# Kernel optimization log

Hardware: AMD Instinct MI355X
Metric: run time of the kernel (lower is better)

Reference implementation:

```python
import jax, jax.numpy as jnp
import numpy as np

N = 100000   # nodes per type
E = 400000   # edges per relation
D = 128      # in_dim == out_dim
H = 4        # heads
DK = D // H  # 32
EPS = 1e-5


def setup_inputs() -> dict:
    key = jax.random.key(0)
    ks = jax.random.split(key, 16)
    s = 1.0 / np.sqrt(D)  # fan-in scaling for stable activations
    inp = {
        "x_drug": jax.random.normal(ks[0], (N, D), jnp.float32),
        "x_dis": jax.random.normal(ks[1], (N, D), jnp.float32),
        "Wp_drug": jax.random.normal(ks[2], (D, D), jnp.float32) * s,
        "bp_drug": jnp.zeros((D,), jnp.float32),
        "Wp_dis": jax.random.normal(ks[3], (D, D), jnp.float32) * s,
        "bp_dis": jnp.zeros((D,), jnp.float32),
        "Wk_r0": jax.random.normal(ks[4], (D, D), jnp.float32) * s,
        "Wv_r0": jax.random.normal(ks[5], (D, D), jnp.float32) * s,
        "Wk_r1": jax.random.normal(ks[6], (D, D), jnp.float32) * s,
        "Wv_r1": jax.random.normal(ks[7], (D, D), jnp.float32) * s,
        "Wu_drug": jax.random.normal(ks[8], (D, D), jnp.float32) * s,
        "bu_drug": jnp.zeros((D,), jnp.float32),
        "Wu_dis": jax.random.normal(ks[9], (D, D), jnp.float32) * s,
        "bu_dis": jnp.zeros((D,), jnp.float32),
        "g_drug": jnp.ones((D,), jnp.float32),
        "be_drug": jnp.zeros((D,), jnp.float32),
        "g_dis": jnp.ones((D,), jnp.float32),
        "be_dis": jnp.zeros((D,), jnp.float32),
        "ei_r0": jax.random.randint(ks[10], (2, E), 0, N, jnp.int32),  # drug -> dis
        "ei_r1": jax.random.randint(ks[11], (2, E), 0, N, jnp.int32),  # dis  -> drug
    }
    return inp


def _rel_attention(h_src_all, h_dst_all, ei, Wk, Wv, n_dst):
    # gather -> per-relation K/V proj -> edge softmax over dst -> scatter-add
    src, dst = ei[0], ei[1]
    h_src = h_src_all[src]                                  # [E, D]
    Q = h_dst_all[dst].reshape(-1, H, DK)                   # [E, H, DK]
    K = (h_src @ Wk).reshape(-1, H, DK)
    V = (h_src @ Wv).reshape(-1, H, DK)
    scores = jnp.sum(Q * K, axis=-1) / np.sqrt(DK)          # [E, H]
    # scatter_softmax over destination groups (numerically stable)
    m = jax.lax.stop_gradient(
        jax.ops.segment_max(scores, dst, num_segments=n_dst))  # [N, H]
    ex = jnp.exp(scores - m[dst])
    ssum = jax.ops.segment_sum(ex, dst, num_segments=n_dst)    # [N, H]
    attn = ex / ssum[dst]                                      # [E, H]
    wV = (V * attn[..., None]).reshape(-1, D)                  # [E, D]
    return jax.ops.segment_sum(wV, dst, num_segments=n_dst)    # [N, D]


def _update(h, agg, Wu, bu, g, be):
    x = h + (agg @ Wu + bu)  # skip + update (dropout=0)
    mu = jnp.mean(x, axis=-1, keepdims=True)
    var = jnp.var(x, axis=-1, keepdims=True)
    ln = (x - mu) * jax.lax.rsqrt(var + EPS) * g + be
    return jax.nn.relu(ln)


def reference(x_drug, x_dis, Wp_drug, bp_drug, Wp_dis, bp_dis,
              Wk_r0, Wv_r0, Wk_r1, Wv_r1,
              Wu_drug, bu_drug, Wu_dis, bu_dis,
              g_drug, be_drug, g_dis, be_dis, ei_r0, ei_r1):
    # type-specific projection
    h_drug = x_drug @ Wp_drug + bp_drug
    h_dis = x_dis @ Wp_dis + bp_dis
    # per-relation attention + intra/inter-type aggregation
    agg_dis = _rel_attention(h_drug, h_dis, ei_r0, Wk_r0, Wv_r0, N)
    agg_drug = _rel_attention(h_dis, h_drug, ei_r1, Wk_r1, Wv_r1, N)
    out_drug = _update(h_drug, agg_drug, Wu_drug, bu_drug, g_drug, be_drug)
    out_dis = _update(h_dis, agg_dis, Wu_dis, bu_dis, g_dis, be_dis)
    return jnp.stack([out_drug, out_dis])  # [2, N, D]
```

## Files before the change

kernel.cpp:

```cpp
#include <hip/hip_runtime.h>
#include <math.h>

#define NN 100000
#define EE 400000
#define DD 128

typedef __attribute__((ext_vector_type(8))) short bf16x8;
typedef __attribute__((ext_vector_type(4))) float f32x4;

#if defined(__has_builtin)
#if __has_builtin(__builtin_amdgcn_fdot2_f32_bf16)
#define HAVE_FDOT2 1
typedef __attribute__((ext_vector_type(2))) __bf16 bf16x2t;
#endif
#endif

__device__ __forceinline__ unsigned short f2bf(float f) {
  unsigned u = __float_as_uint(f);
  u += 0x7FFF + ((u >> 16) & 1);
  return (unsigned short)(u >> 16);
}
__device__ __forceinline__ float bf2f(unsigned short u) {
  return __uint_as_float(((unsigned)u) << 16);
}

__global__ __launch_bounds__(256) void prep_weights(
    const float* __restrict__ Wp_dr, const float* __restrict__ bp_dr,
    const float* __restrict__ Wp_di, const float* __restrict__ bp_di,
    const float* __restrict__ Wu_dr, const float* __restrict__ Wu_di,
    const float* __restrict__ Bk0, const float* __restrict__ Bv0,
    const float* __restrict__ Bk1, const float* __restrict__ Bv1,
    unsigned short* __restrict__ Wpt_dr, unsigned short* __restrict__ Wpt_di,
    unsigned short* __restrict__ Wut_dr, unsigned short* __restrict__ Wut_di,
    unsigned short* __restrict__ Wkt0, float* __restrict__ bk0,
    unsigned short* __restrict__ Wvt0, float* __restrict__ bv0,
    unsigned short* __restrict__ Wkt1, float* __restrict__ bk1,
    unsigned short* __restrict__ Wvt1, float* __restrict__ bv1) {
  const int b = blockIdx.x, t = threadIdx.x;
  if (b < 256) {
    const int id = b * 256 + t;
    const int m = id >> 14, rem = id & 16383, k = rem & 127, c = rem >> 7;
    const float* W = (m == 0) ? Wp_dr : (m == 1) ? Wp_di : (m == 2) ? Wu_dr : Wu_di;
    unsigned short* O = (m == 0) ? Wpt_dr : (m == 1) ? Wpt_di : (m == 2) ? Wut_dr : Wut_di;
    O[c * DD + k] = f2bf(W[(size_t)k * DD + c]);
  } else if (b < 512) {
    const int id = (b - 256) * 256 + t;
    const int m = id >> 14, rem = id & 16383, k = rem & 127, c = rem >> 7;
    const float* A = (m < 2) ? Wp_dr : Wp_di;
    const float* B = (m == 0) ? Bk0 : (m == 1) ? Bv0 : (m == 2) ? Bk1 : Bv1;
    unsigned short* O = (m == 0) ? Wkt0 : (m == 1) ? Wvt0 : (m == 2) ? Wkt1 : Wvt1;
    const float4* a4 = (const float4*)(A + (size_t)k * DD);
    float s = 0.0f;
#pragma unroll 8
    for (int j4 = 0; j4 < 32; ++j4) {
      const float4 av = a4[j4];
      s += av.x * B[(4 * j4 + 0) * DD + c] + av.y * B[(4 * j4 + 1) * DD + c]
         + av.z * B[(4 * j4 + 2) * DD + c] + av.w * B[(4 * j4 + 3) * DD + c];
    }
    O[c * DD + k] = f2bf(s);
  } else {
    const int id = (b - 512) * 256 + t;
    if (id < 512) {
      const int m = id >> 7, c = id & 127;
      const float* bp = (m < 2) ? bp_dr : bp_di;
      const float* B = (m == 0) ? Bk0 : (m == 1) ? Bv0 : (m == 2) ? Bk1 : Bv1;
      float* bo = (m == 0) ? bk0 : (m == 1) ? bv0 : (m == 2) ? bk1 : bv1;
      float s = 0.0f;
#pragma unroll 8
      for (int j = 0; j < DD; ++j) s += bp[j] * B[j * DD + c];
      bo[c] = s;
    }
  }
}

__device__ __forceinline__ void proj_phase(
    const unsigned short* __restrict__ Wt, const float* __restrict__ bias,
    unsigned short* __restrict__ outg, unsigned short* WL, unsigned short* OT,
    const bf16x8* a, int tid, int lane, int wid, int rb) {
  __syncthreads();
#pragma unroll
  for (int i = tid; i < 2048; i += 256) {
    const int L = i * 16;
    *(float4*)((char*)WL + (L ^ (((L >> 8) & 7) << 4))) = ((const float4*)Wt)[i];
  }
  __syncthreads();
  const int lr0 = (lane >> 4) * 4;
  const int trow = wid * 16 + lr0;
#pragma unroll
  for (int ni = 0; ni < 8; ++ni) {
    const int cl = ni * 16 + (lane & 15);
    f32x4 acc = {0.f, 0.f, 0.f, 0.f};
#pragma unroll
    for (int kk = 0; kk < 4; ++kk) {
      int boff = cl * 256 + kk * 64 + (lane >> 4) * 16;
      boff ^= (cl & 7) << 4;
      const bf16x8 bb = *(const bf16x8*)((const char*)WL + boff);
      acc = __builtin_amdgcn_mfma_f32_16x16x32_bf16(a[kk], bb, acc, 0, 0, 0);
    }
    const float bv = bias[cl];
#pragma unroll
    for (int r = 0; r < 4; ++r)
      OT[(trow + r) * DD + cl] = f2bf(acc[r] + bv);
  }
  __syncthreads();
#pragma unroll
  for (int it = 0; it < 4; ++it) {
    const int row = it * 16 + (tid >> 4), c = (tid & 15) * 8;
    if (rb + row < NN)
      *(uint4*)(outg + (size_t)(rb + row) * DD + c) = *(const uint4*)(OT + row * DD + c);
  }
}

__global__ __launch_bounds__(256) void fused_proj(
    const float* __restrict__ x0, const unsigned short* __restrict__ Wpt0,
    const float* __restrict__ bp0, const unsigned short* __restrict__ Wkta,
    const float* __restrict__ bka, const unsigned short* __restrict__ Wvta,
    const float* __restrict__ bva, unsigned short* __restrict__ h0,
    unsigned short* __restrict__ K0, unsigned short* __restrict__ V0,
    const float* __restrict__ x1, const unsigned short* __restrict__ Wpt1,
    const float* __restrict__ bp1, const unsigned short* __restrict__ Wktb,
    const float* __restrict__ bkb, const unsigned short* __restrict__ Wvtb,
    const float* __restrict__ bvb, unsigned short* __restrict__ h1,
    unsigned short* __restrict__ K1, unsigned short* __restrict__ V1, int half) {
  __shared__ unsigned short WL[DD * DD];
  __shared__ unsigned short AL[64 * DD];
  __shared__ unsigned short OT[64 * DD];
  int bid = blockIdx.x;
  const bool second = bid >= half;
  if (second) bid -= half;
  const float* x = second ? x1 : x0;
  const unsigned short* Wpt = second ? Wpt1 : Wpt0;
  const float* bpv = second ? bp1 : bp0;
  const unsigned short* Wkt = second ? Wktb : Wkta;
  const float* bkv = second ? bkb : bka;
  const unsigned short* Wvt = second ? Wvtb : Wvta;
  const float* bvv = second ? bvb : bva;
  unsigned short* h = second ? h1 : h0;
  unsigned short* K = second ? K1 : K0;
  unsigned short* V = second ? V1 : V0;

  const int tid = threadIdx.x, lane = tid & 63, wid = tid >> 6;
  const int rb = bid * 64;
#pragma unroll
  for (int it = 0; it < 8; ++it) {
    const int r = it * 8 + (tid >> 5), c = (tid & 31) * 4;
    unsigned long long pk = 0;
    if (rb + r < NN) {
      const float4 f = *(const float4*)(x + (size_t)(rb + r) * DD + c);
      pk = (unsigned long long)f2bf(f.x) | ((unsigned long long)f2bf(f.y) << 16)
         | ((unsigned long long)f2bf(f.z) << 32) | ((unsigned long long)f2bf(f.w) << 48);
    }
    int L = r * 256 + c * 2;
    L ^= (r & 7) << 4;
    *(unsigned long long*)((char*)AL + L) = pk;
  }
  __syncthreads();
  bf16x8 a[4];
  {
    const int ar = wid * 16 + (lane & 15);
#pragma unroll
    for (int kk = 0; kk < 4; ++kk) {
      int L = ar * 256 + kk * 64 + (lane >> 4) * 16;
      L ^= (ar & 7) << 4;
      a[kk] = *(const bf16x8*)((const char*)AL + L);
    }
  }
  proj_phase(Wpt, bpv, h, WL, OT, a, tid, lane, wid, rb);
  proj_phase(Wkt, bkv, K, WL, OT, a, tid, lane, wid, rb);
  proj_phase(Wvt, bvv, V, WL, OT, a, tid, lane, wid, rb);
}

__global__ __launch_bounds__(256) void update_ln2(
    const unsigned short* __restrict__ hA, const unsigned short* __restrict__ aggA,
    const unsigned short* __restrict__ WutA, const float* __restrict__ buA,
    const float* __restrict__ gA, const float* __restrict__ beA,
    float* __restrict__ outA,
    const unsigned short* __restrict__ hB, const unsigned short* __restrict__ aggB,
    const unsigned short* __restrict__ WutB, const float* __restrict__ buB,
    const float* __restrict__ gB, const float* __restrict__ beB,
    float* __restrict__ outB, int half) {
  __shared__ unsigned short WL[DD * DD];
  __shared__ unsigned short AL[64 * DD];
  __shared__ unsigned short OT[64 * DD];
  int bid = blockIdx.x;
  const bool second = bid >= half;
  if (second) bid -= half;
  const unsigned short* h = second ? hB : hA;
  const unsigned short* agg = second ? aggB : aggA;
  const unsigned short* Wut = second ? WutB : WutA;
  const float* bu = second ? buB : buA;
  const float* g = second ? gB : gA;
  const float* be = second ? beB : beA;
  float* out = second ? outB : outA;

  const int tid = threadIdx.x, lane = tid & 63, wid = tid >> 6;
  const int rb = bid * 64;
#pragma unroll
  for (int it = 0; it < 4; ++it) {
    const int row = it * 16 + (tid >> 4), c = (tid & 15) * 8;
    uint4 va = {0, 0, 0, 0}, vh = {0, 0, 0, 0};
    if (rb + row < NN) {
      va = *(const uint4*)(agg + (size_t)(rb + row) * DD + c);
      vh = *(const uint4*)(h + (size_t)(rb + row) * DD + c);
    }
    int L = row * 256 + c * 2;
    L ^= (row & 7) << 4;
    *(uint4*)((char*)AL + L) = va;
    *(uint4*)(OT + row * DD + c) = vh;
  }
#pragma unroll
  for (int i = tid; i < 2048; i += 256) {
    const int L = i * 16;
    *(float4*)((char*)WL + (L ^ (((L >> 8) & 7) << 4))) = ((const float4*)Wut)[i];
  }
  __syncthreads();
  bf16x8 a[4];
  {
    const int ar = wid * 16 + (lane & 15);
#pragma unroll
    for (int kk = 0; kk < 4; ++kk) {
      int L = ar * 256 + kk * 64 + (lane >> 4) * 16;
      L ^= (ar & 7) << 4;
      a[kk] = *(const bf16x8*)((const char*)AL + L);
    }
  }
  f32x4 acc[8];
  const int lr0 = (lane >> 4) * 4;
  const int trow = wid * 16 + lr0;
#pragma unroll
  for (int ni = 0; ni < 8; ++ni) {
    const int cl = ni * 16 + (lane & 15);
    acc[ni] = (f32x4){0.f, 0.f, 0.f, 0.f};
#pragma unroll
    for (int kk = 0; kk < 4; ++kk) {
      int boff = cl * 256 + kk * 64 + (lane >> 4) * 16;
      boff ^= (cl & 7) << 4;
      const bf16x8 bb = *(const bf16x8*)((const char*)WL + boff);
      acc[ni] = __builtin_amdgcn_mfma_f32_16x16x32_bf16(a[kk], bb, acc[ni], 0, 0, 0);
    }
  }
#pragma unroll
  for (int ni = 0; ni < 8; ++ni) {
    const int cl = ni * 16 + (lane & 15);
    const float bv = bu[cl];
#pragma unroll
    for (int r = 0; r < 4; ++r)
      acc[ni][r] += bf2f(OT[(trow + r) * DD + cl]) + bv;
  }
  float mean[4], inv[4];
#pragma unroll
  for (int r = 0; r < 4; ++r) {
    float s = 0.f, q = 0.f;
#pragma unroll
    for (int ni = 0; ni < 8; ++ni) {
      const float v = acc[ni][r];
      s += v; q += v * v;
    }
    s += __shfl_xor(s, 1); q += __shfl_xor(q, 1);
    s += __shfl_xor(s, 2); q += __shfl_xor(q, 2);
    s += __shfl_xor(s, 4); q += __shfl_xor(q, 4);
    s += __shfl_xor(s, 8); q += __shfl_xor(q, 8);
    const float mu = s * (1.0f / 128.0f);
    mean[r] = mu;
    inv[r] = rsqrtf(q * (1.0f / 128.0f) - mu * mu + 1e-5f);
  }
  __syncthreads();
  float* WLf = (float*)WL;
#pragma unroll
  for (int ni = 0; ni < 8; ++ni) {
    const int cl = ni * 16 + (lane & 15);
    const float gv = g[cl], bev = be[cl];
#pragma unroll
    for (int r = 0; r < 4; ++r)
      WLf[(trow + r) * DD + cl] =
          fmaxf((acc[ni][r] - mean[r]) * inv[r] * gv + bev, 0.0f);
  }
  __syncthreads();
#pragma unroll
  for (int it = 0; it < 8; ++it) {
    const int row = it * 8 + (tid >> 5), c = (tid & 31) * 4;
    if (rb + row < NN)
      *(float4*)(out + (size_t)(rb + row) * DD + c) = *(const float4*)(WLf + row * DD + c);
  }
}

__global__ __launch_bounds__(256) void count_deg2(const int* __restrict__ ei0,
                                                  const int* __restrict__ ei1,
                                                  int* __restrict__ deg) {
  const int e = blockIdx.x * 256 + threadIdx.x;
  if (e >= 2 * EE) return;
  const int d = (e < EE) ? ei0[EE + e] : (NN + ei1[e]);
  atomicAdd(&deg[d], 1);
}

__global__ __launch_bounds__(256) void scan1(const int* __restrict__ deg,
                                             int* __restrict__ excl,
                                             int* __restrict__ partials, int n) {
  __shared__ int ls[256];
  const int b0 = blockIdx.x * 1024;
  const int t = threadIdx.x;
  int v[4];
  int s = 0;
#pragma unroll
  for (int i = 0; i < 4; ++i) {
    const int idx = b0 + t * 4 + i;
    v[i] = (idx < n) ? deg[idx] : 0;
    s += v[i];
  }
  ls[t] = s;
  __syncthreads();
  for (int off = 1; off < 256; off <<= 1) {
    const int x = (t >= off) ? ls[t - off] : 0;
    __syncthreads();
    ls[t] += x;
    __syncthreads();
  }
  int ex = ls[t] - s;
#pragma unroll
  for (int i = 0; i < 4; ++i) {
    const int idx = b0 + t * 4 + i;
    if (idx < n) excl[idx] = ex;
    ex += v[i];
  }
  if (t == 255) partials[blockIdx.x] = ls[255];
}

__global__ __launch_bounds__(256) void scan2(int* __restrict__ partials, int nb) {
  __shared__ int ls[256];
  const int t = threadIdx.x;
  const int v = (t < nb) ? partials[t] : 0;
  ls[t] = v;
  __syncthreads();
  for (int off = 1; off < 256; off <<= 1) {
    const int x = (t >= off) ? ls[t - off] : 0;
    __syncthreads();
    ls[t] += x;
    __syncthreads();
  }
  if (t < nb) partials[t] = ls[t] - v;
}

__global__ __launch_bounds__(256) void scan3(const int* __restrict__ excl,
                                             const int* __restrict__ partials,
                                             int n, int* __restrict__ rowptr,
                                             int* __restrict__ cursor) {
  const int i = blockIdx.x * 256 + threadIdx.x;
  if (i < n) {
    const int v = excl[i] + partials[i >> 10];
    rowptr[i] = v;
    cursor[i] = v;
  }
  if (i == 0) rowptr[n] = 2 * EE;
}

__global__ __launch_bounds__(256) void fill_csr2(const int* __restrict__ ei0,
                                                 const int* __restrict__ ei1,
                                                 int* __restrict__ cursor,
                                                 int* __restrict__ csr_src) {
  const int e = blockIdx.x * 256 + threadIdx.x;
  if (e >= 2 * EE) return;
  int s, d;
  if (e < EE) { s = ei0[e]; d = ei0[EE + e]; }
  else        { s = ei1[e - EE]; d = NN + ei1[e]; }
  const int p = atomicAdd(&cursor[d], 1);
  csr_src[p] = s;
}

__global__ __launch_bounds__(256) void dst_attention(
    const unsigned short* __restrict__ Hq0, const unsigned short* __restrict__ K0,
    const unsigned short* __restrict__ V0, unsigned short* __restrict__ agg0,
    const unsigned short* __restrict__ Hq1, const unsigned short* __restrict__ K1,
    const unsigned short* __restrict__ V1, unsigned short* __restrict__ agg1,
    const int* __restrict__ rowptr, const int* __restrict__ csr_src) {
  const int gw = blockIdx.x * 4 + (threadIdx.x >> 6);
  if (gw >= 2 * NN) return;
  const bool rel1 = gw >= NN;
  const int node = rel1 ? gw - NN : gw;
  const unsigned short* Hq = rel1 ? Hq1 : Hq0;
  const unsigned short* K = rel1 ? K1 : K0;
  const unsigned short* V = rel1 ? V1 : V0;
  unsigned short* agg = rel1 ? agg1 : agg0;

  const int lane = threadIdx.x & 63;
  const int sub = lane & 15;
  const int grp = lane >> 4;
  const int beg = rowptr[gw], end = rowptr[gw + 1];
  const uint4 qu = *(const uint4*)(Hq + (size_t)node * DD + sub * 8);
#if defined(HAVE_FDOT2)
  const bf16x2t q0 = __builtin_bit_cast(bf16x2t, qu.x);
  const bf16x2t q1 = __builtin_bit_cast(bf16x2t, qu.y);
  const bf16x2t q2 = __builtin_bit_cast(bf16x2t, qu.z);
  const bf16x2t q3 = __builtin_bit_cast(bf16x2t, qu.w);
#else
  float qf[8];
  qf[0] = bf2f((unsigned short)qu.x); qf[1] = bf2f((unsigned short)(qu.x >> 16));
  qf[2] = bf2f((unsigned short)qu.y); qf[3] = bf2f((unsigned short)(qu.y >> 16));
  qf[4] = bf2f((unsigned short)qu.z); qf[5] = bf2f((unsigned short)(qu.z >> 16));
  qf[6] = bf2f((unsigned short)qu.w); qf[7] = bf2f((unsigned short)(qu.w >> 16));
#endif
  float av[8] = {0.f, 0.f, 0.f, 0.f, 0.f, 0.f, 0.f, 0.f};
  float lsum = 0.0f;
  for (int i = beg + grp; i < end; i += 4) {
    const int sidx = csr_src[i];
    const uint4 kp = *(const uint4*)(K + (size_t)sidx * DD + sub * 8);
#if defined(HAVE_FDOT2)
    float p = __builtin_amdgcn_fdot2_f32_bf16(__builtin_bit_cast(bf16x2t, kp.x), q0, 0.0f, false);
    p = __builtin_amdgcn_fdot2_f32_bf16(__builtin_bit_cast(bf16x2t, kp.y), q1, p, false);
    p = __builtin_amdgcn_fdot2_f32_bf16(__builtin_bit_cast(bf16x2t, kp.z), q2, p, false);
    p = __builtin_amdgcn_fdot2_f32_bf16(__builtin_bit_cast(bf16x2t, kp.w), q3, p, false);
#else
    float p;
    p  = qf[0] * bf2f((unsigned short)kp.x) + qf[1] * bf2f((unsigned short)(kp.x >> 16));
    p += qf[2] * bf2f((unsigned short)kp.y) + qf[3] * bf2f((unsigned short)(kp.y >> 16));
    p += qf[4] * bf2f((unsigned short)kp.z) + qf[5] * bf2f((unsigned short)(kp.z >> 16));
    p += qf[6] * bf2f((unsigned short)kp.w) + qf[7] * bf2f((unsigned short)(kp.w >> 16));
#endif
    p += __shfl_xor(p, 1);
    p += __shfl_xor(p, 2);
    const float wgt = __expf(p * 0.17677669529663689f);
    const uint4 vp = *(const uint4*)(V + (size_t)sidx * DD + sub * 8);
    lsum += wgt;
    av[0] += wgt * __uint_as_float(vp.x << 16);
    av[1] += wgt * __uint_as_float(vp.x & 0xFFFF0000u);
    av[2] += wgt * __uint_as_float(vp.y << 16);
    av[3] += wgt * __uint_as_float(vp.y & 0xFFFF0000u);
    av[4] += wgt * __uint_as_float(vp.z << 16);
    av[5] += wgt * __uint_as_float(vp.z & 0xFFFF0000u);
    av[6] += wgt * __uint_as_float(vp.w << 16);
    av[7] += wgt * __uint_as_float(vp.w & 0xFFFF0000u);
  }
#pragma unroll
  for (int d = 0; d < 8; ++d) {
    av[d] += __shfl_xor(av[d], 16);
    av[d] += __shfl_xor(av[d], 32);
  }
  lsum += __shfl_xor(lsum, 16);
  lsum += __shfl_xor(lsum, 32);
  if (grp == 0) {
    const float invl = (lsum > 0.0f) ? (1.0f / lsum) : 0.0f;
    uint4 o;
    o.x = (unsigned)f2bf(av[0] * invl) | ((unsigned)f2bf(av[1] * invl) << 16);
    o.y = (unsigned)f2bf(av[2] * invl) | ((unsigned)f2bf(av[3] * invl) << 16);
    o.z = (unsigned)f2bf(av[4] * invl) | ((unsigned)f2bf(av[5] * invl) << 16);
    o.w = (unsigned)f2bf(av[6] * invl) | ((unsigned)f2bf(av[7] * invl) << 16);
    *(uint4*)(agg + (size_t)node * DD + sub * 8) = o;
  }
}

extern "C" void kernel_launch(void* const* d_in, const int* in_sizes, int n_in,
                              void* d_out, int out_size, void* d_ws, size_t ws_size,
                              hipStream_t stream) {
  const float* x_drug  = (const float*)d_in[0];
  const float* x_dis   = (const float*)d_in[1];
  const float* Wp_drug = (const float*)d_in[2];
  const float* bp_drug = (const float*)d_in[3];
  const float* Wp_dis  = (const float*)d_in[4];
  const float* bp_dis  = (const float*)d_in[5];
  const float* Wk_r0   = (const float*)d_in[6];
  const float* Wv_r0   = (const float*)d_in[7];
  const float* Wk_r1   = (const float*)d_in[8];
  const float* Wv_r1   = (const float*)d_in[9];
  const float* Wu_drug = (const float*)d_in[10];
  const float* bu_drug = (const float*)d_in[11];
  const float* Wu_dis  = (const float*)d_in[12];
  const float* bu_dis  = (const float*)d_in[13];
  const float* g_drug  = (const float*)d_in[14];
  const float* be_drug = (const float*)d_in[15];
  const float* g_dis   = (const float*)d_in[16];
  const float* be_dis  = (const float*)d_in[17];
  const int* ei_r0     = (const int*)d_in[18];
  const int* ei_r1     = (const int*)d_in[19];

  float* out = (float*)d_out;
  float* out_drug = out;
  float* out_dis  = out + (size_t)NN * DD;

  const size_t ND = (size_t)NN * DD;
  char* w = (char*)d_ws;
  unsigned short* Kr0  = (unsigned short*)w; w += ND * 2;
  unsigned short* Vr0  = (unsigned short*)w; w += ND * 2;
  unsigned short* Kr1  = (unsigned short*)w; w += ND * 2;
  unsigned short* Vr1  = (unsigned short*)w; w += ND * 2;
  unsigned short* agdr = (unsigned short*)w; w += ND * 2;
  unsigned short* agdi = (unsigned short*)w; w += ND * 2;
  unsigned short* hb_dr = (unsigned short*)w; w += ND * 2;
  unsigned short* hb_di = (unsigned short*)w; w += ND * 2;
  unsigned short* Wpt_dr = (unsigned short*)w; w += DD * DD * 2;
  unsigned short* Wpt_di = (unsigned short*)w; w += DD * DD * 2;
  unsigned short* Wut_dr = (unsigned short*)w; w += DD * DD * 2;
  unsigned short* Wut_di = (unsigned short*)w; w += DD * DD * 2;
  unsigned short* Wkt0 = (unsigned short*)w; w += DD * DD * 2;
  unsigned short* Wvt0 = (unsigned short*)w; w += DD * DD * 2;
  unsigned short* Wkt1 = (unsigned short*)w; w += DD * DD * 2;
  unsigned short* Wvt1 = (unsigned short*)w; w += DD * DD * 2;
  float* bk0 = (float*)w; w += DD * 4;
  float* bv0 = (float*)w; w += DD * 4;
  float* bk1 = (float*)w; w += DD * 4;
  float* bv1 = (float*)w; w += DD * 4;
  int* deg      = (int*)w; w += 2 * NN * 4;
  int* excl     = (int*)w; w += 2 * NN * 4;
  int* rowptr   = (int*)w; w += (2 * NN + 1) * 4;
  int* cursor   = (int*)w; w += 2 * NN * 4;
  int* partials = (int*)w; w += 256 * 4;
  int* csr_src  = (int*)w; w += 2 * EE * 4;

  const int gemm_blocks = (NN + 63) / 64;
  const int edge_blocks2 = (2 * EE + 255) / 256;
  const int nchunks = (2 * NN + 1023) / 1024;
  const int n256 = (2 * NN + 255) / 256;
  const int attn_blocks = (2 * NN + 3) / 4;
  dim3 b256(256);

  prep_weights<<<514, b256, 0, stream>>>(
      Wp_drug, bp_drug, Wp_dis, bp_dis, Wu_drug, Wu_dis,
      Wk_r0, Wv_r0, Wk_r1, Wv_r1,
      Wpt_dr, Wpt_di, Wut_dr, Wut_di,
      Wkt0, bk0, Wvt0, bv0, Wkt1, bk1, Wvt1, bv1);

  fused_proj<<<2 * gemm_blocks, b256, 0, stream>>>(
      x_drug, Wpt_dr, bp_drug, Wkt0, bk0, Wvt0, bv0, hb_dr, Kr0, Vr0,
      x_dis,  Wpt_di, bp_dis,  Wkt1, bk1, Wvt1, bv1, hb_di, Kr1, Vr1,
      gemm_blocks);

  hipMemsetAsync(deg, 0, 2 * NN * sizeof(int), stream);
  count_deg2<<<edge_blocks2, b256, 0, stream>>>(ei_r0, ei_r1, deg);
  scan1<<<nchunks, b256, 0, stream>>>(deg, excl, partials, 2 * NN);
  scan2<<<1, b256, 0, stream>>>(partials, nchunks);
  scan3<<<n256, b256, 0, stream>>>(excl, partials, 2 * NN, rowptr, cursor);
  fill_csr2<<<edge_blocks2, b256, 0, stream>>>(ei_r0, ei_r1, cursor, csr_src);

  dst_attention<<<attn_blocks, b256, 0, stream>>>(
      hb_di, Kr0, Vr0, agdi,
      hb_dr, Kr1, Vr1, agdr,
      rowptr, csr_src);

  update_ln2<<<2 * gemm_blocks, b256, 0, stream>>>(
      hb_dr, agdr, Wut_dr, bu_drug, g_drug, be_drug, out_drug,
      hb_di, agdi, Wut_di, bu_dis,  g_dis,  be_dis,  out_dis,
      gemm_blocks);
}
```

Baseline: 345.8 us.

## Drop LDS staging in projection and update GEMMs, feed MFMA from global

The projection and update kernels no longer stage x, weights and outputs through shared memory with barriers. Each lane now loads its MFMA fragments directly from global memory. The operand order is swapped so that weights are the A operand, which lets each lane write four contiguous outputs of one row and reduce LayerNorm statistics with two shuffles. The projection kernel now handles 128 rows per block, with two row fragments per wave sharing each weight fragment load. This removes LDS traffic, syncs and the shared-memory occupancy limit. In exchange, weight fragments are re-read from global/L2 for every wave.

Result: slower. 393.4 us (+13.8%).

```diff
diff --git a/kernel.cpp b/kernel.cpp
--- a/kernel.cpp
+++ b/kernel.cpp
@@ -7,6 +7,7 @@
 
 typedef __attribute__((ext_vector_type(8))) short bf16x8;
 typedef __attribute__((ext_vector_type(4))) float f32x4;
+typedef __attribute__((ext_vector_type(4))) short s16x4;
 
 #if defined(__has_builtin)
 #if __has_builtin(__builtin_amdgcn_fdot2_f32_bf16)
@@ -73,41 +74,56 @@
   }
 }
 
-__device__ __forceinline__ void proj_phase(
+__device__ __forceinline__ void load_xfrag(const float* __restrict__ x,
+                                           int row, bool valid, int lane,
+                                           bf16x8* a) {
+  if (valid) {
+    const float* xr = x + (size_t)row * DD + (lane >> 4) * 8;
+#pragma unroll
+    for (int kk = 0; kk < 4; ++kk) {
+      const float4 f0 = *(const float4*)(xr + kk * 32);
+      const float4 f1 = *(const float4*)(xr + kk * 32 + 4);
+      a[kk][0] = (short)f2bf(f0.x); a[kk][1] = (short)f2bf(f0.y);
+      a[kk][2] = (short)f2bf(f0.z); a[kk][3] = (short)f2bf(f0.w);
+      a[kk][4] = (short)f2bf(f1.x); a[kk][5] = (short)f2bf(f1.y);
+      a[kk][6] = (short)f2bf(f1.z); a[kk][7] = (short)f2bf(f1.w);
+    }
+  } else {
+#pragma unroll
+    for (int kk = 0; kk < 4; ++kk)
+#pragma unroll
+      for (int j = 0; j < 8; ++j) a[kk][j] = 0;
+  }
+}
+
+__device__ __forceinline__ void proj_phase2(
     const unsigned short* __restrict__ Wt, const float* __restrict__ bias,
-    unsigned short* __restrict__ outg, unsigned short* WL, unsigned short* OT,
-    const bf16x8* a, int tid, int lane, int wid, int rb) {
-  __syncthreads();
-#pragma unroll
-  for (int i = tid; i < 2048; i += 256) {
-    const int L = i * 16;
-    *(float4*)((char*)WL + (L ^ (((L >> 8) & 7) << 4))) = ((const float4*)Wt)[i];
-  }
-  __syncthreads();
-  const int lr0 = (lane >> 4) * 4;
-  const int trow = wid * 16 + lr0;
+    unsigned short* __restrict__ outg, const bf16x8* a1, const bf16x8* a2,
+    int lane, int row1, int row2, bool v1, bool v2) {
+  const int colb = (lane >> 4) * 4;
 #pragma unroll
   for (int ni = 0; ni < 8; ++ni) {
-    const int cl = ni * 16 + (lane & 15);
-    f32x4 acc = {0.f, 0.f, 0.f, 0.f};
+    f32x4 acc1 = {0.f, 0.f, 0.f, 0.f}, acc2 = {0.f, 0.f, 0.f, 0.f};
 #pragma unroll
     for (int kk = 0; kk < 4; ++kk) {
-      int boff = cl * 256 + kk * 64 + (lane >> 4) * 16;
-      boff ^= (cl & 7) << 4;
-      const bf16x8 bb = *(const bf16x8*)((const char*)WL + boff);
-      acc = __builtin_amdgcn_mfma_f32_16x16x32_bf16(a[kk], bb, acc, 0, 0, 0);
-    }
-    const float bv = bias[cl];
-#pragma unroll
-    for (int r = 0; r < 4; ++r)
-      OT[(trow + r) * DD + cl] = f2bf(acc[r] + bv);
-  }
-  __syncthreads();
-#pragma unroll
-  for (int it = 0; it < 4; ++it) {
-    const int row = it * 16 + (tid >> 4), c = (tid & 15) * 8;
-    if (rb + row < NN)
-      *(uint4*)(outg + (size_t)(rb + row) * DD + c) = *(const uint4*)(OT + row * DD + c);
+      const bf16x8 wf = *(const bf16x8*)(
+          Wt + (size_t)(ni * 16 + (lane & 15)) * DD + kk * 32 + (lane >> 4) * 8);
+      acc1 = __builtin_amdgcn_mfma_f32_16x16x32_bf16(wf, a1[kk], acc1, 0, 0, 0);
+      acc2 = __builtin_amdgcn_mfma_f32_16x16x32_bf16(wf, a2[kk], acc2, 0, 0, 0);
+    }
+    const float4 bv = *(const float4*)(bias + ni * 16 + colb);
+    if (v1) {
+      s16x4 o;
+      o.x = (short)f2bf(acc1[0] + bv.x); o.y = (short)f2bf(acc1[1] + bv.y);
+      o.z = (short)f2bf(acc1[2] + bv.z); o.w = (short)f2bf(acc1[3] + bv.w);
+      *(s16x4*)(outg + (size_t)row1 * DD + ni * 16 + colb) = o;
+    }
+    if (v2) {
+      s16x4 o;
+      o.x = (short)f2bf(acc2[0] + bv.x); o.y = (short)f2bf(acc2[1] + bv.y);
+      o.z = (short)f2bf(acc2[2] + bv.z); o.w = (short)f2bf(acc2[3] + bv.w);
+      *(s16x4*)(outg + (size_t)row2 * DD + ni * 16 + colb) = o;
+    }
   }
 }
 
@@ -122,9 +138,6 @@
     const float* __restrict__ bkb, const unsigned short* __restrict__ Wvtb,
     const float* __restrict__ bvb, unsigned short* __restrict__ h1,
     unsigned short* __restrict__ K1, unsigned short* __restrict__ V1, int half) {
-  __shared__ unsigned short WL[DD * DD];
-  __shared__ unsigned short AL[64 * DD];
-  __shared__ unsigned short OT[64 * DD];
   int bid = blockIdx.x;
   const bool second = bid >= half;
   if (second) bid -= half;
@@ -140,34 +153,15 @@
   unsigned short* V = second ? V1 : V0;
 
   const int tid = threadIdx.x, lane = tid & 63, wid = tid >> 6;
-  const int rb = bid * 64;
-#pragma unroll
-  for (int it = 0; it < 8; ++it) {
-    const int r = it * 8 + (tid >> 5), c = (tid & 31) * 4;
-    unsigned long long pk = 0;
-    if (rb + r < NN) {
-      const float4 f = *(const float4*)(x + (size_t)(rb + r) * DD + c);
-      pk = (unsigned long long)f2bf(f.x) | ((unsigned long long)f2bf(f.y) << 16)
-         | ((unsigned long long)f2bf(f.z) << 32) | ((unsigned long long)f2bf(f.w) << 48);
-    }
-    int L = r * 256 + c * 2;
-    L ^= (r & 7) << 4;
-    *(unsigned long long*)((char*)AL + L) = pk;
-  }
-  __syncthreads();
-  bf16x8 a[4];
-  {
-    const int ar = wid * 16 + (lane & 15);
-#pragma unroll
-    for (int kk = 0; kk < 4; ++kk) {
-      int L = ar * 256 + kk * 64 + (lane >> 4) * 16;
-      L ^= (ar & 7) << 4;
-      a[kk] = *(const bf16x8*)((const char*)AL + L);
-    }
-  }
-  proj_phase(Wpt, bpv, h, WL, OT, a, tid, lane, wid, rb);
-  proj_phase(Wkt, bkv, K, WL, OT, a, tid, lane, wid, rb);
-  proj_phase(Wvt, bvv, V, WL, OT, a, tid, lane, wid, rb);
+  const int row1 = bid * 128 + wid * 32 + (lane & 15);
+  const int row2 = row1 + 16;
+  const bool v1 = row1 < NN, v2 = row2 < NN;
+  bf16x8 a1[4], a2[4];
+  load_xfrag(x, row1, v1, lane, a1);
+  load_xfrag(x, row2, v2, lane, a2);
+  proj_phase2(Wpt, bpv, h, a1, a2, lane, row1, row2, v1, v2);
+  proj_phase2(Wkt, bkv, K, a1, a2, lane, row1, row2, v1, v2);
+  proj_phase2(Wvt, bvv, V, a1, a2, lane, row1, row2, v1, v2);
 }
 
 __global__ __launch_bounds__(256) void update_ln2(
@@ -179,9 +173,6 @@
     const unsigned short* __restrict__ WutB, const float* __restrict__ buB,
     const float* __restrict__ gB, const float* __restrict__ beB,
     float* __restrict__ outB, int half) {
-  __shared__ unsigned short WL[DD * DD];
-  __shared__ unsigned short AL[64 * DD];
-  __shared__ unsigned short OT[64 * DD];
   int bid = blockIdx.x;
   const bool second = bid >= half;
   if (second) bid -= half;
@@ -194,93 +185,62 @@
   float* out = second ? outB : outA;
 
   const int tid = threadIdx.x, lane = tid & 63, wid = tid >> 6;
-  const int rb = bid * 64;
-#pragma unroll
-  for (int it = 0; it < 4; ++it) {
-    const int row = it * 16 + (tid >> 4), c = (tid & 15) * 8;
-    uint4 va = {0, 0, 0, 0}, vh = {0, 0, 0, 0};
-    if (rb + row < NN) {
-      va = *(const uint4*)(agg + (size_t)(rb + row) * DD + c);
-      vh = *(const uint4*)(h + (size_t)(rb + row) * DD + c);
-    }
-    int L = row * 256 + c * 2;
-    L ^= (row & 7) << 4;
-    *(uint4*)((char*)AL + L) = va;
-    *(uint4*)(OT + row * DD + c) = vh;
-  }
-#pragma unroll
-  for (int i = tid; i < 2048; i += 256) {
-    const int L = i * 16;
-    *(float4*)((char*)WL + (L ^ (((L >> 8) & 7) << 4))) = ((const float4*)Wut)[i];
-  }
-  __syncthreads();
+  const int row = bid * 64 + wid * 16 + (lane & 15);
+  const bool valid = row < NN;
+  const int colb = (lane >> 4) * 4;
+
   bf16x8 a[4];
-  {
-    const int ar = wid * 16 + (lane & 15);
+  if (valid) {
+#pragma unroll
+    for (int kk = 0; kk < 4; ++kk)
+      a[kk] = *(const bf16x8*)(agg + (size_t)row * DD + kk * 32 + (lane >> 4) * 8);
+  } else {
+#pragma unroll
+    for (int kk = 0; kk < 4; ++kk)
+#pragma unroll
+      for (int j = 0; j < 8; ++j) a[kk][j] = 0;
+  }
+  f32x4 acc[8];
+#pragma unroll
+  for (int ni = 0; ni < 8; ++ni) {
+    acc[ni] = (f32x4){0.f, 0.f, 0.f, 0.f};
 #pragma unroll
     for (int kk = 0; kk < 4; ++kk) {
-      int L = ar * 256 + kk * 64 + (lane >> 4) * 16;
-      L ^= (ar & 7) << 4;
-      a[kk] = *(const bf16x8*)((const char*)AL + L);
-    }
-  }
-  f32x4 acc[8];
-  const int lr0 = (lane >> 4) * 4;
-  const int trow = wid * 16 + lr0;
+      const bf16x8 wf = *(const bf16x8*)(
+          Wut + (size_t)(ni * 16 + (lane & 15)) * DD + kk * 32 + (lane >> 4) * 8);
+      acc[ni] = __builtin_amdgcn_mfma_f32_16x16x32_bf16(wf, a[kk], acc[ni], 0, 0, 0);
+    }
+  }
+  float s = 0.f, q = 0.f;
 #pragma unroll
   for (int ni = 0; ni < 8; ++ni) {
-    const int cl = ni * 16 + (lane & 15);
-    acc[ni] = (f32x4){0.f, 0.f, 0.f, 0.f};
-#pragma unroll
-    for (int kk = 0; kk < 4; ++kk) {
-      int boff = cl * 256 + kk * 64 + (lane >> 4) * 16;
-      boff ^= (cl & 7) << 4;
-      const bf16x8 bb = *(const bf16x8*)((const char*)WL + boff);
-      acc[ni] = __builtin_amdgcn_mfma_f32_16x16x32_bf16(a[kk], bb, acc[ni], 0, 0, 0);
-    }
-  }
+    const int c = ni * 16 + colb;
+    const float4 bv = *(const float4*)(bu + c);
+    s16x4 hv = {0, 0, 0, 0};
+    if (valid) hv = *(const s16x4*)(h + (size_t)row * DD + c);
+    acc[ni][0] += bf2f((unsigned short)hv.x) + bv.x;
+    acc[ni][1] += bf2f((unsigned short)hv.y) + bv.y;
+    acc[ni][2] += bf2f((unsigned short)hv.z) + bv.z;
+    acc[ni][3] += bf2f((unsigned short)hv.w) + bv.w;
+#pragma unroll
+    for (int r = 0; r < 4; ++r) { s += acc[ni][r]; q += acc[ni][r] * acc[ni][r]; }
+  }
+  s += __shfl_xor(s, 16); q += __shfl_xor(q, 16);
+  s += __shfl_xor(s, 32); q += __shfl_xor(q, 32);
+  const float mu = s * (1.0f / 128.0f);
+  const float inv = rsqrtf(q * (1.0f / 128.0f) - mu * mu + 1e-5f);
+  if (!valid) return;
 #pragma unroll
   for (int ni = 0; ni < 8; ++ni) {
-    const int cl = ni * 16 + (lane & 15);
-    const float bv = bu[cl];
-#pragma unroll
-    for (int r = 0; r < 4; ++r)
-      acc[ni][r] += bf2f(OT[(trow + r) * DD + cl]) + bv;
-  }
-  float mean[4], inv[4];
-#pragma unroll
-  for (int r = 0; r < 4; ++r) {
-    float s = 0.f, q = 0.f;
-#pragma unroll
-    for (int ni = 0; ni < 8; ++ni) {
-      const float v = acc[ni][r];
-      s += v; q += v * v;
-    }
-    s += __shfl_xor(s, 1); q += __shfl_xor(q, 1);
-    s += __shfl_xor(s, 2); q += __shfl_xor(q, 2);
-    s += __shfl_xor(s, 4); q += __shfl_xor(q, 4);
-    s += __shfl_xor(s, 8); q += __shfl_xor(q, 8);
-    const float mu = s * (1.0f / 128.0f);
-    mean[r] = mu;
-    inv[r] = rsqrtf(q * (1.0f / 128.0f) - mu * mu + 1e-5f);
-  }
-  __syncthreads();
-  float* WLf = (float*)WL;
-#pragma unroll
-  for (int ni = 0; ni < 8; ++ni) {
-    const int cl = ni * 16 + (lane & 15);
-    const float gv = g[cl], bev = be[cl];
-#pragma unroll
-    for (int r = 0; r < 4; ++r)
-      WLf[(trow + r) * DD + cl] =
-          fmaxf((acc[ni][r] - mean[r]) * inv[r] * gv + bev, 0.0f);
-  }
-  __syncthreads();
-#pragma unroll
-  for (int it = 0; it < 8; ++it) {
-    const int row = it * 8 + (tid >> 5), c = (tid & 31) * 4;
-    if (rb + row < NN)
-      *(float4*)(out + (size_t)(rb + row) * DD + c) = *(const float4*)(WLf + row * DD + c);
+    const int c = ni * 16 + colb;
+    const float4 gv = *(const float4*)(g + c);
+    const float4 bev = *(const float4*)(be + c);
+    float4 o;
+    o.x = fmaxf((acc[ni][0] - mu) * inv * gv.x + bev.x, 0.0f);
+    o.y = fmaxf((acc[ni][1] - mu) * inv * gv.y + bev.y, 0.0f);
+    o.z = fmaxf((acc[ni][2] - mu) * inv * gv.z + bev.z, 0.0f);
+    o.w = fmaxf((acc[ni][3] - mu) * inv * gv.w + bev.w, 0.0f);
+    *(float4*)(out + (size_t)row * DD + c) = o;
   }
 }
 
@@ -504,7 +464,8 @@
   int* partials = (int*)w; w += 256 * 4;
   int* csr_src  = (int*)w; w += 2 * EE * 4;
 
-  const int gemm_blocks = (NN + 63) / 64;
+  const int proj_blocks = (NN + 127) / 128;
+  const int upd_blocks = (NN + 63) / 64;
   const int edge_blocks2 = (2 * EE + 255) / 256;
   const int nchunks = (2 * NN + 1023) / 1024;
   const int n256 = (2 * NN + 255) / 256;
@@ -517,10 +478,10 @@
       Wpt_dr, Wpt_di, Wut_dr, Wut_di,
       Wkt0, bk0, Wvt0, bv0, Wkt1, bk1, Wvt1, bv1);
 
-  fused_proj<<<2 * gemm_blocks, b256, 0, stream>>>(
+  fused_proj<<<2 * proj_blocks, b256, 0, stream>>>(
       x_drug, Wpt_dr, bp_drug, Wkt0, bk0, Wvt0, bv0, hb_dr, Kr0, Vr0,
       x_dis,  Wpt_di, bp_dis,  Wkt1, bk1, Wvt1, bv1, hb_di, Kr1, Vr1,
-      gemm_blocks);
+      proj_blocks);
 
   hipMemsetAsync(deg, 0, 2 * NN * sizeof(int), stream);
   count_deg2<<<edge_blocks2, b256, 0, stream>>>(ei_r0, ei_r1, deg);
@@ -534,8 +495,8 @@
       hb_dr, Kr1, Vr1, agdr,
       rowptr, csr_src);
 
-  update_ln2<<<2 * gemm_blocks, b256, 0, stream>>>(
+  update_ln2<<<2 * upd_blocks, b256, 0, stream>>>(
       hb_dr, agdr, Wut_dr, bu_drug, g_drug, be_drug, out_drug,
       hb_di, agdi, Wut_di, bu_dis,  g_dis,  be_dis,  out_dis,
-      gemm_blocks);
-}
+      upd_blocks);
+}
```
